# Performance work log

Measured on AMD Instinct MI355X. Metric: run time of the kernel, lower is better.

The kernel has to match this reference:

```python
import jax, jax.numpy as jnp
import numpy as np

B, S, D, H = 4, 2048, 1024, 16
HD = D // H


def setup_inputs() -> dict:
    key = jax.random.key(0)
    ks = jax.random.split(key, 10)
    x = jax.random.normal(ks[0], (B, S, D), dtype=jnp.float32)
    mask = jnp.zeros((B, 1, 1, S), dtype=jnp.float32)  # 1 = masked, 0 = keep
    sc = 1.0 / np.sqrt(D)
    wq = jax.random.normal(ks[1], (D, D), dtype=jnp.float32) * sc
    wk = jax.random.normal(ks[2], (D, D), dtype=jnp.float32) * sc
    wv = jax.random.normal(ks[3], (D, D), dtype=jnp.float32) * sc
    wo = jax.random.normal(ks[4], (D, D), dtype=jnp.float32) * sc
    bq = jnp.zeros((D,), jnp.float32)
    bk = jnp.zeros((D,), jnp.float32)
    bv = jnp.zeros((D,), jnp.float32)
    bo = jnp.zeros((D,), jnp.float32)
    return {"x": x, "mask": mask, "wq": wq, "bq": bq, "wk": wk, "bk": bk,
            "wv": wv, "bv": bv, "wo": wo, "bo": bo}


def _split_heads(t):
    # (B, S, D) -> (B, H, S, HD)
    return t.reshape(B, -1, H, HD).transpose(0, 2, 1, 3)


def reference(x, mask, wq, bq, wk, bk, wv, bv, wo, bo):
    q = _split_heads(x @ wq + bq)
    k = _split_heads(x @ wk + bk)
    v = _split_heads(x @ wv + bv)
    # scaled dot-product attention (TF tutorial convention: mask*-1e9 added)
    scores = jnp.einsum("bhqd,bhkd->bhqk", q, k) / jnp.sqrt(jnp.float32(HD))
    scores = scores + mask * -1e9
    attn_weights = jax.nn.softmax(scores, axis=-1)  # (B, H, Sq, Sk)
    attn = jnp.einsum("bhqk,bhkd->bhqd", attn_weights, v)
    attn = attn.transpose(0, 2, 1, 3).reshape(B, -1, D)
    out = attn @ wo + bo
    return out, attn_weights
```

## Files before the change

kernel.cpp:

```cpp
#include <hip/hip_runtime.h>
#include <hip/hip_bf16.h>

#define S_LEN  2048
#define DMODEL 1024
#define NHEAD  16
#define HDIM   64
#define BSZ    4

#define C_SCORE  0.18033688f
#define C_MASK  -1.4426950e9f

typedef __bf16 bf16_t;
typedef __bf16 bf16x8 __attribute__((ext_vector_type(8)));
typedef __bf16 bf16x4 __attribute__((ext_vector_type(4)));
typedef float  f32x4  __attribute__((ext_vector_type(4)));

typedef __attribute__((address_space(1))) void as1_void;
typedef __attribute__((address_space(3))) void as3_void;

__device__ __forceinline__ f32x4 mfma16(bf16x8 a, bf16x8 b, f32x4 c) {
    return __builtin_amdgcn_mfma_f32_16x16x32_bf16(a, b, c, 0, 0, 0);
}

__global__ __launch_bounds__(256) void cvt_x_kernel(const float* __restrict__ x,
                                                    bf16_t* __restrict__ xb, int n4) {
    int i = blockIdx.x * 256 + threadIdx.x;
    int stride = gridDim.x * 256;
    for (; i < n4; i += stride) {
        float4 v = ((const float4*)x)[i];
        bf16x4 t = { (bf16_t)v.x, (bf16_t)v.y, (bf16_t)v.z, (bf16_t)v.w };
        ((bf16x4*)xb)[i] = t;
    }
}

__global__ __launch_bounds__(256) void cvt_wT_kernel(const float* __restrict__ w,
                                                     bf16_t* __restrict__ wT) {
    __shared__ bf16_t t[64][65];
    const int bx = blockIdx.x * 64;
    const int by = blockIdx.y * 64;
    const int tx = threadIdx.x & 63, ty = threadIdx.x >> 6;
    #pragma unroll
    for (int rr = 0; rr < 64; rr += 4)
        t[tx][rr + ty] = (bf16_t)w[(size_t)(bx + rr + ty) * DMODEL + by + tx];
    __syncthreads();
    #pragma unroll
    for (int rr = 0; rr < 64; rr += 4)
        wT[(size_t)(by + rr + ty) * DMODEL + bx + tx] = t[rr + ty][tx];
}

__global__ __launch_bounds__(256) void transpose_v(const bf16_t* __restrict__ V,
                                                   bf16_t* __restrict__ Vt) {
    __shared__ __attribute__((aligned(16))) bf16_t t[64][72];
    const int bh = blockIdx.y;
    const int s0 = blockIdx.x * 64;
    const int tid = threadIdx.x;
    const bf16_t* Vb = V + (size_t)bh * S_LEN * HDIM;
    bf16_t* Vo = Vt + (size_t)bh * HDIM * S_LEN;
    #pragma unroll
    for (int p = 0; p < 2; ++p) {
        const int sl = p * 32 + (tid >> 3);
        const int c8 = (tid & 7) * 8;
        bf16x8 v = *(const bf16x8*)(Vb + (size_t)(s0 + sl) * HDIM + c8);
        #pragma unroll
        for (int j = 0; j < 8; ++j) t[c8 + j][sl] = v[j];
    }
    __syncthreads();
    #pragma unroll
    for (int p = 0; p < 2; ++p) {
        const int dl = p * 32 + (tid >> 3);
        const int s8 = (tid & 7) * 8;
        bf16x8 v = *(const bf16x8*)(&t[dl][s8]);
        *(bf16x8*)(Vo + (size_t)dl * S_LEN + s0 + s8) = v;
    }
}

template <int MODE>
__global__ __launch_bounds__(256) void gemm_bt(const bf16_t* __restrict__ A,
                                               const bf16_t* __restrict__ Bt,
                                               const float* __restrict__ b0,
                                               const float* __restrict__ b1,
                                               const float* __restrict__ b2,
                                               bf16_t* __restrict__ o0,
                                               bf16_t* __restrict__ o1,
                                               bf16_t* __restrict__ o2,
                                               float* __restrict__ of) {
    constexpr int GK = 1024;
    __shared__ __attribute__((aligned(16))) bf16_t As[128 * 32];
    __shared__ __attribute__((aligned(16))) bf16_t Bs[128 * 32];

    const int tid  = threadIdx.x;
    const int wave = tid >> 6, lane = tid & 63;
    const int col16 = lane & 15, g = lane >> 4;
    const int wr = wave >> 1, wc = wave & 1;
    const int bn0 = blockIdx.x * 128, bm0 = blockIdx.y * 128;

    const int r4 = tid >> 2;
    const int c8 = (tid & 3) * 8;

    f32x4 acc[4][4] = {};

    for (int k0 = 0; k0 < GK; k0 += 32) {
        __syncthreads();
        #pragma unroll
        for (int i = 0; i < 2; ++i) {
            __builtin_amdgcn_global_load_lds(
                (const as1_void*)(A + (size_t)(bm0 + i * 64 + r4) * GK + k0 + c8),
                (as3_void*)(As + (i * 64 + wave * 16) * 32), 16, 0, 0);
            __builtin_amdgcn_global_load_lds(
                (const as1_void*)(Bt + (size_t)(bn0 + i * 64 + r4) * GK + k0 + c8),
                (as3_void*)(Bs + (i * 64 + wave * 16) * 32), 16, 0, 0);
        }
        __syncthreads();

        bf16x8 af[4], bfr[4];
        #pragma unroll
        for (int i = 0; i < 4; ++i) {
            af[i]  = *(const bf16x8*)(As + (wr * 64 + i * 16 + col16) * 32 + g * 8);
            bfr[i] = *(const bf16x8*)(Bs + (wc * 64 + i * 16 + col16) * 32 + g * 8);
        }
        #pragma unroll
        for (int mi = 0; mi < 4; ++mi)
            #pragma unroll
            for (int ni = 0; ni < 4; ++ni)
                acc[mi][ni] = mfma16(af[mi], bfr[ni], acc[mi][ni]);
    }

    #pragma unroll
    for (int ni = 0; ni < 4; ++ni) {
        const int gn = bn0 + wc * 64 + ni * 16 + col16;
        if (MODE == 0) {
            const int proj = bn0 >> 10;
            const float* bias = proj == 0 ? b0 : (proj == 1 ? b1 : b2);
            bf16_t* outp      = proj == 0 ? o0 : (proj == 1 ? o1 : o2);
            const int n1 = gn & 1023, h = n1 >> 6, hd = n1 & 63;
            const float bv = bias[n1];
            #pragma unroll
            for (int mi = 0; mi < 4; ++mi)
                #pragma unroll
                for (int r = 0; r < 4; ++r) {
                    const int gm = bm0 + wr * 64 + mi * 16 + g * 4 + r;
                    const int b = gm >> 11, s = gm & 2047;
                    outp[(((size_t)b * NHEAD + h) * S_LEN + s) * HDIM + hd] =
                        (bf16_t)(acc[mi][ni][r] + bv);
                }
        } else {
            const float bv = b0[gn];
            #pragma unroll
            for (int mi = 0; mi < 4; ++mi)
                #pragma unroll
                for (int r = 0; r < 4; ++r) {
                    const int gm = bm0 + wr * 64 + mi * 16 + g * 4 + r;
                    of[(size_t)gm * DMODEL + gn] = acc[mi][ni][r] + bv;
                }
        }
    }
}

__global__ __launch_bounds__(256, 2) void attn_fused(const bf16_t* __restrict__ Q,
                                                     const bf16_t* __restrict__ K,
                                                     const bf16_t* __restrict__ Vt,
                                                     const float* __restrict__ mask,
                                                     float* __restrict__ attnW,
                                                     bf16_t* __restrict__ ctx) {
    __shared__ __attribute__((aligned(16))) bf16_t Ks[2][64][64];
    __shared__ __attribute__((aligned(16))) bf16_t Vs[2][64][64];
    __shared__ __attribute__((aligned(16))) float  Pl[4][32][64];

    const int tid = threadIdx.x, wave = tid >> 6, lane = tid & 63;
    const int col16 = lane & 15, g = lane >> 4;
    const int r7 = col16 & 7;

    const int lin = blockIdx.y * 16 + blockIdx.x;
    const int logical = (lin & 7) * 128 + (lin >> 3);
    const int bh = logical >> 4, qt = logical & 15;
    const int b = bh >> 4, h = bh & 15;
    const int q0 = qt * 128 + wave * 32;

    const bf16_t* Qb = Q + (size_t)bh * S_LEN * HDIM;
    const bf16_t* Kb = K + (size_t)bh * S_LEN * HDIM;
    const bf16_t* Vb = Vt + (size_t)bh * HDIM * S_LEN;
    const float* mp = mask + (size_t)b * S_LEN;

    const int srow  = lane >> 3;
    const int sunit = (lane & 7) ^ srow;

    auto stageK = [&](int buf, int it) {
        const int kk0 = it << 6;
        #pragma unroll
        for (int i2 = 0; i2 < 2; ++i2) {
            const int i = wave * 2 + i2;
            __builtin_amdgcn_global_load_lds(
                (const as1_void*)(Kb + (size_t)(kk0 + i * 8 + srow) * HDIM + sunit * 8),
                (as3_void*)(&Ks[buf][i * 8][0]), 16, 0, 0);
        }
    };
    auto stageV = [&](int buf, int it) {
        const int kk0 = it << 6;
        #pragma unroll
        for (int i2 = 0; i2 < 2; ++i2) {
            const int i = wave * 2 + i2;
            __builtin_amdgcn_global_load_lds(
                (const as1_void*)(Vb + (size_t)(i * 8 + srow) * S_LEN + kk0 + sunit * 8),
                (as3_void*)(&Vs[buf][i * 8][0]), 16, 0, 0);
        }
    };
    auto kfrag = [&](int buf, int nj, int kh) {
        return *(const bf16x8*)(&Ks[buf][nj * 16 + col16][(((kh * 4 + g) ^ r7) * 8)]);
    };
    auto vfrag = [&](int buf, int nd, int kh) {
        return *(const bf16x8*)(&Vs[buf][nd * 16 + col16][(((kh * 4 + g) ^ r7) * 8)]);
    };

    bf16x8 qa[2][2];
    #pragma unroll
    for (int hh = 0; hh < 2; ++hh)
        #pragma unroll
        for (int kh = 0; kh < 2; ++kh)
            qa[hh][kh] = *(const bf16x8*)(Qb + (size_t)(q0 + hh * 16 + col16) * HDIM +
                                          kh * 32 + g * 8);

    f32x4 lacc[2] = {};

    stageK(0, 0);
    asm volatile("s_waitcnt vmcnt(0)" ::: "memory");
    __builtin_amdgcn_sched_barrier(0);
    __builtin_amdgcn_s_barrier();

    for (int it = 0; it < 32; ++it) {
        const int kk0 = it << 6, cur = it & 1;
        f32x4 mvr[4];
        #pragma unroll
        for (int nj = 0; nj < 4; ++nj) mvr[nj] = ((const f32x4*)(mp + kk0 + nj * 16))[g];
        if (it < 31) stageK(cur ^ 1, it + 1);
        #pragma unroll
        for (int nj = 0; nj < 4; ++nj) {
            const bf16x8 kf0 = kfrag(cur, nj, 0);
            const bf16x8 kf1 = kfrag(cur, nj, 1);
            f32x4 t0 = {0.f, 0.f, 0.f, 0.f}, t1 = {0.f, 0.f, 0.f, 0.f};
            t0 = mfma16(kf0, qa[0][0], t0);
            t0 = mfma16(kf1, qa[0][1], t0);
            t1 = mfma16(kf0, qa[1][0], t1);
            t1 = mfma16(kf1, qa[1][1], t1);
            #pragma unroll
            for (int r = 0; r < 4; ++r) {
                const float mm = mvr[nj][r] * C_MASK;
                lacc[0][r] += exp2f(fmaf(t0[r], C_SCORE, mm));
                lacc[1][r] += exp2f(fmaf(t1[r], C_SCORE, mm));
            }
        }
        asm volatile("s_waitcnt vmcnt(0)" ::: "memory");
        __builtin_amdgcn_sched_barrier(0);
        __builtin_amdgcn_s_barrier();
    }

    float crow[2];
    #pragma unroll
    for (int hh = 0; hh < 2; ++hh) {
        float lr = (lacc[hh][0] + lacc[hh][1]) + (lacc[hh][2] + lacc[hh][3]);
        lr += __shfl_xor(lr, 16);
        lr += __shfl_xor(lr, 32);
        crow[hh] = -__log2f(lr);
    }

    f32x4 o[2][4] = {};
    float* awbase = attnW + ((size_t)bh * S_LEN + q0) * S_LEN;

    stageK(0, 0);
    stageV(0, 0);
    asm volatile("s_waitcnt vmcnt(0)" ::: "memory");
    __builtin_amdgcn_sched_barrier(0);
    __builtin_amdgcn_s_barrier();

    for (int it = 0; it < 32; ++it) {
        const int kk0 = it << 6, cur = it & 1;
        f32x4 mvr[4];
        #pragma unroll
        for (int nj = 0; nj < 4; ++nj) mvr[nj] = ((const f32x4*)(mp + kk0 + nj * 16))[g];
        if (it < 31) { stageK(cur ^ 1, it + 1); stageV(cur ^ 1, it + 1); }

        #pragma unroll
        for (int nj = 0; nj < 4; ++nj) {
            const bf16x8 kf0 = kfrag(cur, nj, 0);
            const bf16x8 kf1 = kfrag(cur, nj, 1);
            f32x4 t0 = {0.f, 0.f, 0.f, 0.f}, t1 = {0.f, 0.f, 0.f, 0.f};
            t0 = mfma16(kf0, qa[0][0], t0);
            t0 = mfma16(kf1, qa[0][1], t0);
            t1 = mfma16(kf0, qa[1][0], t1);
            t1 = mfma16(kf1, qa[1][1], t1);
            f32x4 pn0, pn1;
            #pragma unroll
            for (int r = 0; r < 4; ++r) {
                const float mm = mvr[nj][r] * C_MASK;
                pn0[r] = exp2f(fmaf(t0[r], C_SCORE, mm + crow[0]));
                pn1[r] = exp2f(fmaf(t1[r], C_SCORE, mm + crow[1]));
            }
            const int pw = ((nj * 4 + g) ^ r7) * 4;
            *(f32x4*)(&Pl[wave][col16][pw])      = pn0;
            *(f32x4*)(&Pl[wave][16 + col16][pw]) = pn1;
        }

        #pragma unroll
        for (int j = 0; j < 8; ++j) {
            const int row = j * 4 + (lane >> 4);
            const int u = lane & 15;
            const f32x4 v = *(const f32x4*)(&Pl[wave][row][((u ^ (row & 7)) * 4)]);
            __builtin_nontemporal_store(v, (f32x4*)(awbase + (size_t)row * S_LEN + kk0 + u * 4));
        }

        #pragma unroll
        for (int hh = 0; hh < 2; ++hh)
            #pragma unroll
            for (int kh = 0; kh < 2; ++kh) {
                const int u0 = kh * 8 + g * 2;
                const f32x4 a0 = *(const f32x4*)(&Pl[wave][hh * 16 + col16][((u0 ^ r7) * 4)]);
                const f32x4 a1 = *(const f32x4*)(&Pl[wave][hh * 16 + col16][(((u0 + 1) ^ r7) * 4)]);
                bf16x8 pa;
                #pragma unroll
                for (int j = 0; j < 4; ++j) {
                    pa[j]     = (bf16_t)a0[j];
                    pa[4 + j] = (bf16_t)a1[j];
                }
                #pragma unroll
                for (int nd = 0; nd < 4; ++nd)
                    o[hh][nd] = mfma16(vfrag(cur, nd, kh), pa, o[hh][nd]);
            }

        asm volatile("s_waitcnt vmcnt(8)" ::: "memory");
        __builtin_amdgcn_sched_barrier(0);
        __builtin_amdgcn_s_barrier();
    }

    #pragma unroll
    for (int hh = 0; hh < 2; ++hh) {
        bf16_t* cp = ctx + ((size_t)b * S_LEN + q0 + hh * 16 + col16) * DMODEL + h * HDIM;
        #pragma unroll
        for (int nd = 0; nd < 4; ++nd) {
            bf16x4 cv;
            #pragma unroll
            for (int r = 0; r < 4; ++r) cv[r] = (bf16_t)o[hh][nd][r];
            *(bf16x4*)(cp + nd * 16 + g * 4) = cv;
        }
    }
}

extern "C" void kernel_launch(void* const* d_in, const int* in_sizes, int n_in,
                              void* d_out, int out_size, void* d_ws, size_t ws_size,
                              hipStream_t stream) {
    const float* x    = (const float*)d_in[0];
    const float* mask = (const float*)d_in[1];
    const float* wq   = (const float*)d_in[2];
    const float* bq   = (const float*)d_in[3];
    const float* wk   = (const float*)d_in[4];
    const float* bk   = (const float*)d_in[5];
    const float* wv   = (const float*)d_in[6];
    const float* bv   = (const float*)d_in[7];
    const float* wo   = (const float*)d_in[8];
    const float* bo   = (const float*)d_in[9];

    const size_t nX = (size_t)BSZ * S_LEN * DMODEL;
    const size_t nW = (size_t)DMODEL * DMODEL;

    char* ws = (char*)d_ws;
    size_t off = 0;
    bf16_t* xb     = (bf16_t*)(ws + off); off += nX * 2;
    bf16_t* wqkvT  = (bf16_t*)(ws + off); off += 3 * nW * 2;
    bf16_t* woT    = (bf16_t*)(ws + off); off += nW * 2;
    bf16_t* qbh    = (bf16_t*)(ws + off); off += nX * 2;
    bf16_t* kbh    = (bf16_t*)(ws + off); off += nX * 2;
    bf16_t* vrow   = (bf16_t*)(ws + off); off += nX * 2;
    bf16_t* vtb    = (bf16_t*)(ws + off); off += nX * 2;
    bf16_t* ctx    = (bf16_t*)(ws + off); off += nX * 2;
    if (ws_size < off) return;

    float* outp  = (float*)d_out;
    float* attnW = outp + nX;

    cvt_x_kernel<<<4096, 256, 0, stream>>>(x, xb, (int)(nX / 4));
    cvt_wT_kernel<<<dim3(16, 16), 256, 0, stream>>>(wq, wqkvT);
    cvt_wT_kernel<<<dim3(16, 16), 256, 0, stream>>>(wk, wqkvT + nW);
    cvt_wT_kernel<<<dim3(16, 16), 256, 0, stream>>>(wv, wqkvT + 2 * nW);
    cvt_wT_kernel<<<dim3(16, 16), 256, 0, stream>>>(wo, woT);

    gemm_bt<0><<<dim3(24, 64), 256, 0, stream>>>(xb, wqkvT, bq, bk, bv,
                                                 qbh, kbh, vrow, nullptr);
    transpose_v<<<dim3(32, 64), 256, 0, stream>>>(vrow, vtb);

    attn_fused<<<dim3(16, 64), 256, 0, stream>>>(qbh, kbh, vtb, mask, attnW, ctx);

    gemm_bt<2><<<dim3(8, 64), 256, 0, stream>>>(ctx, woT, bo, nullptr, nullptr,
                                                nullptr, nullptr, nullptr, outp);
}
```

Baseline: 403.6 us.

## Process two query tiles per block, folding second tile's row-sum pass into first output pass

Each block now handles two 128-row query tiles, so there are half as many blocks. The row-sum pass for the second tile is computed inside the first tile's probability/output pass, reusing the same staged K tiles. The scaled mask is also preloaded into LDS once per block. This removes one full K sweep per pair of tiles and avoids repeated global mask reads, at the cost of more registers, more LDS, and fewer blocks for occupancy.

```diff
diff --git a/kernel.cpp b/kernel.cpp
--- a/kernel.cpp
+++ b/kernel.cpp
@@ -165,21 +165,32 @@
     __shared__ __attribute__((aligned(16))) bf16_t Ks[2][64][64];
     __shared__ __attribute__((aligned(16))) bf16_t Vs[2][64][64];
     __shared__ __attribute__((aligned(16))) float  Pl[4][32][64];
+    __shared__ __attribute__((aligned(16))) float  Ml[S_LEN];
 
     const int tid = threadIdx.x, wave = tid >> 6, lane = tid & 63;
     const int col16 = lane & 15, g = lane >> 4;
     const int r7 = col16 & 7;
 
-    const int lin = blockIdx.y * 16 + blockIdx.x;
-    const int logical = (lin & 7) * 128 + (lin >> 3);
-    const int bh = logical >> 4, qt = logical & 15;
+    const int lin = blockIdx.x;
+    const int logical = (lin & 7) * 64 + (lin >> 3);
+    const int bh = logical >> 3, pp = logical & 7;
     const int b = bh >> 4, h = bh & 15;
-    const int q0 = qt * 128 + wave * 32;
+    const int qA = pp * 256 + wave * 32;
+    const int qB = pp * 256 + 128 + wave * 32;
 
     const bf16_t* Qb = Q + (size_t)bh * S_LEN * HDIM;
     const bf16_t* Kb = K + (size_t)bh * S_LEN * HDIM;
     const bf16_t* Vb = Vt + (size_t)bh * HDIM * S_LEN;
     const float* mp = mask + (size_t)b * S_LEN;
+
+    #pragma unroll
+    for (int i = 0; i < 2; ++i) {
+        const int idx = i * 256 + tid;
+        f32x4 v = ((const f32x4*)mp)[idx];
+        #pragma unroll
+        for (int r = 0; r < 4; ++r) v[r] *= C_MASK;
+        *(f32x4*)(&Ml[idx * 4]) = v;
+    }
 
     const int srow  = lane >> 3;
     const int sunit = (lane & 7) ^ srow;
@@ -211,41 +222,41 @@
         return *(const bf16x8*)(&Vs[buf][nd * 16 + col16][(((kh * 4 + g) ^ r7) * 8)]);
     };
 
-    bf16x8 qa[2][2];
+    bf16x8 qa0[2][2], qa1[2][2];
     #pragma unroll
     for (int hh = 0; hh < 2; ++hh)
         #pragma unroll
-        for (int kh = 0; kh < 2; ++kh)
-            qa[hh][kh] = *(const bf16x8*)(Qb + (size_t)(q0 + hh * 16 + col16) * HDIM +
-                                          kh * 32 + g * 8);
+        for (int kh = 0; kh < 2; ++kh) {
+            qa0[hh][kh] = *(const bf16x8*)(Qb + (size_t)(qA + hh * 16 + col16) * HDIM +
+                                           kh * 32 + g * 8);
+            qa1[hh][kh] = *(const bf16x8*)(Qb + (size_t)(qB + hh * 16 + col16) * HDIM +
+                                           kh * 32 + g * 8);
+        }
 
     f32x4 lacc[2] = {};
-
     stageK(0, 0);
-    asm volatile("s_waitcnt vmcnt(0)" ::: "memory");
-    __builtin_amdgcn_sched_barrier(0);
-    __builtin_amdgcn_s_barrier();
+    __syncthreads();
 
     for (int it = 0; it < 32; ++it) {
         const int kk0 = it << 6, cur = it & 1;
+        if (it < 31) stageK(cur ^ 1, it + 1);
         f32x4 mvr[4];
         #pragma unroll
-        for (int nj = 0; nj < 4; ++nj) mvr[nj] = ((const f32x4*)(mp + kk0 + nj * 16))[g];
-        if (it < 31) stageK(cur ^ 1, it + 1);
+        for (int nj = 0; nj < 4; ++nj)
+            mvr[nj] = *(const f32x4*)(&Ml[kk0 + nj * 16 + g * 4]);
         #pragma unroll
         for (int nj = 0; nj < 4; ++nj) {
             const bf16x8 kf0 = kfrag(cur, nj, 0);
             const bf16x8 kf1 = kfrag(cur, nj, 1);
             f32x4 t0 = {0.f, 0.f, 0.f, 0.f}, t1 = {0.f, 0.f, 0.f, 0.f};
-            t0 = mfma16(kf0, qa[0][0], t0);
-            t0 = mfma16(kf1, qa[0][1], t0);
-            t1 = mfma16(kf0, qa[1][0], t1);
-            t1 = mfma16(kf1, qa[1][1], t1);
+            t0 = mfma16(kf0, qa0[0][0], t0);
+            t0 = mfma16(kf1, qa0[0][1], t0);
+            t1 = mfma16(kf0, qa0[1][0], t1);
+            t1 = mfma16(kf1, qa0[1][1], t1);
             #pragma unroll
             for (int r = 0; r < 4; ++r) {
-                const float mm = mvr[nj][r] * C_MASK;
-                lacc[0][r] += exp2f(fmaf(t0[r], C_SCORE, mm));
-                lacc[1][r] += exp2f(fmaf(t1[r], C_SCORE, mm));
+                lacc[0][r] += exp2f(fmaf(t0[r], C_SCORE, mvr[nj][r]));
+                lacc[1][r] += exp2f(fmaf(t1[r], C_SCORE, mvr[nj][r]));
             }
         }
         asm volatile("s_waitcnt vmcnt(0)" ::: "memory");
@@ -253,17 +264,18 @@
         __builtin_amdgcn_s_barrier();
     }
 
-    float crow[2];
+    float crow0[2];
     #pragma unroll
     for (int hh = 0; hh < 2; ++hh) {
         float lr = (lacc[hh][0] + lacc[hh][1]) + (lacc[hh][2] + lacc[hh][3]);
         lr += __shfl_xor(lr, 16);
         lr += __shfl_xor(lr, 32);
-        crow[hh] = -__log2f(lr);
+        crow0[hh] = -__log2f(lr);
+        lacc[hh] = (f32x4){0.f, 0.f, 0.f, 0.f};
     }
 
     f32x4 o[2][4] = {};
-    float* awbase = attnW + ((size_t)bh * S_LEN + q0) * S_LEN;
+    float* awbase = attnW + ((size_t)bh * S_LEN + qA) * S_LEN;
 
     stageK(0, 0);
     stageV(0, 0);
@@ -273,26 +285,34 @@
 
     for (int it = 0; it < 32; ++it) {
         const int kk0 = it << 6, cur = it & 1;
+        if (it < 31) { stageK(cur ^ 1, it + 1); stageV(cur ^ 1, it + 1); }
         f32x4 mvr[4];
         #pragma unroll
-        for (int nj = 0; nj < 4; ++nj) mvr[nj] = ((const f32x4*)(mp + kk0 + nj * 16))[g];
-        if (it < 31) { stageK(cur ^ 1, it + 1); stageV(cur ^ 1, it + 1); }
+        for (int nj = 0; nj < 4; ++nj)
+            mvr[nj] = *(const f32x4*)(&Ml[kk0 + nj * 16 + g * 4]);
 
         #pragma unroll
         for (int nj = 0; nj < 4; ++nj) {
             const bf16x8 kf0 = kfrag(cur, nj, 0);
             const bf16x8 kf1 = kfrag(cur, nj, 1);
-            f32x4 t0 = {0.f, 0.f, 0.f, 0.f}, t1 = {0.f, 0.f, 0.f, 0.f};
-            t0 = mfma16(kf0, qa[0][0], t0);
-            t0 = mfma16(kf1, qa[0][1], t0);
-            t1 = mfma16(kf0, qa[1][0], t1);
-            t1 = mfma16(kf1, qa[1][1], t1);
+            f32x4 s0 = {0.f, 0.f, 0.f, 0.f}, s1 = {0.f, 0.f, 0.f, 0.f};
+            f32x4 u0 = {0.f, 0.f, 0.f, 0.f}, u1 = {0.f, 0.f, 0.f, 0.f};
+            s0 = mfma16(kf0, qa0[0][0], s0);
+            s0 = mfma16(kf1, qa0[0][1], s0);
+            s1 = mfma16(kf0, qa0[1][0], s1);
+            s1 = mfma16(kf1, qa0[1][1], s1);
+            u0 = mfma16(kf0, qa1[0][0], u0);
+            u0 = mfma16(kf1, qa1[0][1], u0);
+            u1 = mfma16(kf0, qa1[1][0], u1);
+            u1 = mfma16(kf1, qa1[1][1], u1);
             f32x4 pn0, pn1;
             #pragma unroll
             for (int r = 0; r < 4; ++r) {
-                const float mm = mvr[nj][r] * C_MASK;
-                pn0[r] = exp2f(fmaf(t0[r], C_SCORE, mm + crow[0]));
-                pn1[r] = exp2f(fmaf(t1[r], C_SCORE, mm + crow[1]));
+                const float mm = mvr[nj][r];
+                pn0[r] = exp2f(fmaf(s0[r], C_SCORE, mm + crow0[0]));
+                pn1[r] = exp2f(fmaf(s1[r], C_SCORE, mm + crow0[1]));
+                lacc[0][r] += exp2f(fmaf(u0[r], C_SCORE, mm));
+                lacc[1][r] += exp2f(fmaf(u1[r], C_SCORE, mm));
             }
             const int pw = ((nj * 4 + g) ^ r7) * 4;
             *(f32x4*)(&Pl[wave][col16][pw])      = pn0;
@@ -311,9 +331,9 @@
         for (int hh = 0; hh < 2; ++hh)
             #pragma unroll
             for (int kh = 0; kh < 2; ++kh) {
-                const int u0 = kh * 8 + g * 2;
-                const f32x4 a0 = *(const f32x4*)(&Pl[wave][hh * 16 + col16][((u0 ^ r7) * 4)]);
-                const f32x4 a1 = *(const f32x4*)(&Pl[wave][hh * 16 + col16][(((u0 + 1) ^ r7) * 4)]);
+                const int u0i = kh * 8 + g * 2;
+                const f32x4 a0 = *(const f32x4*)(&Pl[wave][hh * 16 + col16][((u0i ^ r7) * 4)]);
+                const f32x4 a1 = *(const f32x4*)(&Pl[wave][hh * 16 + col16][(((u0i + 1) ^ r7) * 4)]);
                 bf16x8 pa;
                 #pragma unroll
                 for (int j = 0; j < 4; ++j) {
@@ -330,9 +350,99 @@
         __builtin_amdgcn_s_barrier();
     }
 
+    float crow1[2];
     #pragma unroll
     for (int hh = 0; hh < 2; ++hh) {
-        bf16_t* cp = ctx + ((size_t)b * S_LEN + q0 + hh * 16 + col16) * DMODEL + h * HDIM;
+        float lr = (lacc[hh][0] + lacc[hh][1]) + (lacc[hh][2] + lacc[hh][3]);
+        lr += __shfl_xor(lr, 16);
+        lr += __shfl_xor(lr, 32);
+        crow1[hh] = -__log2f(lr);
+    }
+
+    #pragma unroll
+    for (int hh = 0; hh < 2; ++hh) {
+        bf16_t* cp = ctx + ((size_t)b * S_LEN + qA + hh * 16 + col16) * DMODEL + h * HDIM;
+        #pragma unroll
+        for (int nd = 0; nd < 4; ++nd) {
+            bf16x4 cv;
+            #pragma unroll
+            for (int r = 0; r < 4; ++r) cv[r] = (bf16_t)o[hh][nd][r];
+            *(bf16x4*)(cp + nd * 16 + g * 4) = cv;
+        }
+        o[hh][0] = o[hh][1] = o[hh][2] = o[hh][3] = (f32x4){0.f, 0.f, 0.f, 0.f};
+    }
+
+    awbase = attnW + ((size_t)bh * S_LEN + qB) * S_LEN;
+
+    stageK(0, 0);
+    stageV(0, 0);
+    asm volatile("s_waitcnt vmcnt(0)" ::: "memory");
+    __builtin_amdgcn_sched_barrier(0);
+    __builtin_amdgcn_s_barrier();
+
+    for (int it = 0; it < 32; ++it) {
+        const int kk0 = it << 6, cur = it & 1;
+        if (it < 31) { stageK(cur ^ 1, it + 1); stageV(cur ^ 1, it + 1); }
+        f32x4 mvr[4];
+        #pragma unroll
+        for (int nj = 0; nj < 4; ++nj)
+            mvr[nj] = *(const f32x4*)(&Ml[kk0 + nj * 16 + g * 4]);
+
+        #pragma unroll
+        for (int nj = 0; nj < 4; ++nj) {
+            const bf16x8 kf0 = kfrag(cur, nj, 0);
+            const bf16x8 kf1 = kfrag(cur, nj, 1);
+            f32x4 t0 = {0.f, 0.f, 0.f, 0.f}, t1 = {0.f, 0.f, 0.f, 0.f};
+            t0 = mfma16(kf0, qa1[0][0], t0);
+            t0 = mfma16(kf1, qa1[0][1], t0);
+            t1 = mfma16(kf0, qa1[1][0], t1);
+            t1 = mfma16(kf1, qa1[1][1], t1);
+            f32x4 pn0, pn1;
+            #pragma unroll
+            for (int r = 0; r < 4; ++r) {
+                const float mm = mvr[nj][r];
+                pn0[r] = exp2f(fmaf(t0[r], C_SCORE, mm + crow1[0]));
+                pn1[r] = exp2f(fmaf(t1[r], C_SCORE, mm + crow1[1]));
+            }
+            const int pw = ((nj * 4 + g) ^ r7) * 4;
+            *(f32x4*)(&Pl[wave][col16][pw])      = pn0;
+            *(f32x4*)(&Pl[wave][16 + col16][pw]) = pn1;
+        }
+
+        #pragma unroll
+        for (int j = 0; j < 8; ++j) {
+            const int row = j * 4 + (lane >> 4);
+            const int u = lane & 15;
+            const f32x4 v = *(const f32x4*)(&Pl[wave][row][((u ^ (row & 7)) * 4)]);
+            __builtin_nontemporal_store(v, (f32x4*)(awbase + (size_t)row * S_LEN + kk0 + u * 4));
+        }
+
+        #pragma unroll
+        for (int hh = 0; hh < 2; ++hh)
+            #pragma unroll
+            for (int kh = 0; kh < 2; ++kh) {
+                const int u0i = kh * 8 + g * 2;
+                const f32x4 a0 = *(const f32x4*)(&Pl[wave][hh * 16 + col16][((u0i ^ r7) * 4)]);
+                const f32x4 a1 = *(const f32x4*)(&Pl[wave][hh * 16 + col16][(((u0i + 1) ^ r7) * 4)]);
+                bf16x8 pa;
+                #pragma unroll
+                for (int j = 0; j < 4; ++j) {
+                    pa[j]     = (bf16_t)a0[j];
+                    pa[4 + j] = (bf16_t)a1[j];
+                }
+                #pragma unroll
+                for (int nd = 0; nd < 4; ++nd)
+                    o[hh][nd] = mfma16(vfrag(cur, nd, kh), pa, o[hh][nd]);
+            }
+
+        asm volatile("s_waitcnt vmcnt(8)" ::: "memory");
+        __builtin_amdgcn_sched_barrier(0);
+        __builtin_amdgcn_s_barrier();
+    }
+
+    #pragma unroll
+    for (int hh = 0; hh < 2; ++hh) {
+        bf16_t* cp = ctx + ((size_t)b * S_LEN + qB + hh * 16 + col16) * DMODEL + h * HDIM;
         #pragma unroll
         for (int nd = 0; nd < 4; ++nd) {
             bf16x4 cv;
@@ -385,7 +495,7 @@
                                                  qbh, kbh, vrow, nullptr);
     transpose_v<<<dim3(32, 64), 256, 0, stream>>>(vrow, vtb);
 
-    attn_fused<<<dim3(16, 64), 256, 0, stream>>>(qbh, kbh, vtb, mask, attnW, ctx);
+    attn_fused<<<512, 256, 0, stream>>>(qbh, kbh, vtb, mask, attnW, ctx);
 
     gemm_bt<2><<<dim3(8, 64), 256, 0, stream>>>(ctx, woT, bo, nullptr, nullptr,
                                                 nullptr, nullptr, nullptr, outp);
```

Result: faster. 382.7 us (-5.2%).
